# Kernel tuning notes

Hardware: AMD Instinct MI355X
Metric: run time of the kernel (lower is better)

## Reference

```python
import jax, jax.numpy as jnp
import numpy as np
import math

H = 128      # hidden_channels
R = 32       # num_rbf
N = 4096     # atoms
E = 65536    # edges
CU = 4.5     # cutoff_upper (cutoff_lower = 0)
ALPHA = 5.0 / CU
MEANS = jnp.linspace(math.exp(-CU), 1.0, R, dtype=jnp.float32)
BETA = jnp.float32((2.0 / R * (1.0 - math.exp(-CU))) ** -2)
EPS = 1e-5


def _ln(x, g, b):
    mu = x.mean(-1, keepdims=True)
    var = ((x - mu) ** 2).mean(-1, keepdims=True)
    return (x - mu) * jax.lax.rsqrt(var + EPS) * g + b


def setup_inputs() -> dict:
    key = jax.random.key(0)
    ks = jax.random.split(key, 20)
    f32 = jnp.float32

    def w(i, shape):
        return jax.random.normal(ks[i], shape, f32) / np.float32(np.sqrt(shape[-1]))

    return {
        "edge_vec": jax.random.normal(ks[0], (E, 3), f32) * 1.5,
        "emb_w": w(1, (128, H)),
        "emb2_w": w(2, (H, 2 * H)), "emb2_b": jnp.zeros((H,), f32),
        "dp1_w": w(3, (H, R)), "dp1_b": jnp.zeros((H,), f32),
        "dp2_w": w(4, (H, R)), "dp2_b": jnp.zeros((H,), f32),
        "dp3_w": w(5, (H, R)), "dp3_b": jnp.zeros((H,), f32),
        "lt0_w": w(6, (H, H)), "lt1_w": w(7, (H, H)), "lt2_w": w(8, (H, H)),
        "ls0_w": w(9, (2 * H, H)), "ls0_b": jnp.zeros((2 * H,), f32),
        "ls1_w": w(10, (3 * H, 2 * H)), "ls1_b": jnp.zeros((3 * H,), f32),
        "init_g": jnp.ones((H,), f32), "init_b": jnp.zeros((H,), f32),
        "lin_w": w(11, (H, 3 * H)), "lin_b": jnp.zeros((H,), f32),
        "outn_g": jnp.ones((3 * H,), f32), "outn_b": jnp.zeros((3 * H,), f32),
        "ol1_w": w(12, (H // 2, H)), "ol1_b": jnp.zeros((H // 2,), f32),
        "ol2_w": w(13, (1, H // 2)), "ol2_b": jnp.zeros((1,), f32),
        "z": jax.random.randint(ks[14], (N,), 0, 128, dtype=jnp.int32),
        "edge_index": jax.random.randint(ks[15], (2, E), 0, N, dtype=jnp.int32),
    }


def reference(edge_vec, emb_w, emb2_w, emb2_b, dp1_w, dp1_b, dp2_w, dp2_b,
              dp3_w, dp3_b, lt0_w, lt1_w, lt2_w, ls0_w, ls0_b, ls1_w, ls1_b,
              init_g, init_b, lin_w, lin_b, outn_g, outn_b, ol1_w, ol1_b,
              ol2_w, ol2_b, z, edge_index):
    n = z.shape[0]
    src, dst = edge_index[0], edge_index[1]

    d = jnp.sqrt((edge_vec ** 2).sum(-1))                 # (E,)
    vn = edge_vec / d[:, None]                             # unit edge vectors
    cut = jnp.where(d < CU, 0.5 * (jnp.cos(jnp.pi * d / CU) + 1.0), 0.0)
    # expnorm RBF
    rbf = cut[:, None] * jnp.exp(-BETA * (jnp.exp(-ALPHA * d)[:, None] - MEANS) ** 2)  # (E,R)

    # atomic-number message Zij = emb2(cat(emb(z_i), emb(z_j)))
    zpair = jnp.concatenate([emb_w[z[src]], emb_w[z[dst]]], -1)  # (E,2H)
    zij = zpair @ emb2_w.T + emb2_b                              # (E,H)
    c = cut[:, None] * zij                                       # cutoff * Zij, (E,H)

    w1 = (rbf @ dp1_w.T + dp1_b) * c    # scalar channel weights (E,H)
    w2 = (rbf @ dp2_w.T + dp2_b) * c
    w3 = (rbf @ dp3_w.T + dp3_b) * c

    eye = jnp.eye(3, dtype=edge_vec.dtype)
    zero = jnp.zeros_like(vn[:, 0])
    skew = jnp.stack([zero, -vn[:, 2], vn[:, 1],
                      vn[:, 2], zero, -vn[:, 0],
                      -vn[:, 1], vn[:, 0], zero], 1).reshape(-1, 3, 3)  # (E,3,3)
    outer = vn[:, :, None] * vn[:, None, :]
    sym = outer - ((vn ** 2).sum(-1) / 3.0)[:, None, None] * eye        # traceless sym (E,3,3)

    seg = lambda a: jax.ops.segment_sum(a, src, num_segments=n)
    I0 = seg(w1)[:, :, None, None] * eye                                # (N,H,3,3)
    A0 = seg(w2[:, :, None, None] * skew[:, None, :, :])                # (N,H,3,3)
    S0 = seg(w3[:, :, None, None] * sym[:, None, :, :])                 # (N,H,3,3)

    tn = ((I0 + A0 + S0) ** 2).sum((-2, -1))                            # tensor_norm, (N,H)
    nrm = _ln(tn, init_g, init_b)
    h = jax.nn.silu(nrm @ ls0_w.T + ls0_b)
    scal = jax.nn.silu(h @ ls1_w.T + ls1_b).reshape(n, H, 3)            # per-channel gates

    I1 = jnp.einsum('nhxy,gh->ngxy', I0, lt0_w) * scal[..., 0][..., None, None]
    A1 = jnp.einsum('nhxy,gh->ngxy', A0, lt1_w) * scal[..., 1][..., None, None]
    S1 = jnp.einsum('nhxy,gh->ngxy', S0, lt2_w) * scal[..., 2][..., None, None]

    x = jnp.concatenate([(I1 ** 2).sum((-2, -1)),
                         (A1 ** 2).sum((-2, -1)),
                         (S1 ** 2).sum((-2, -1))], -1)                  # (N,3H)
    x = _ln(x, outn_g, outn_b)
    s1 = x @ lin_w.T + lin_b
    s2 = jax.nn.silu(s1) @ ol1_w.T + ol1_b
    s3 = jax.nn.silu(s2) @ ol2_w.T + ol2_b                              # per-atom energy (N,1)
    return s3
```

## Files before the change

### kernel.cpp

```cpp
#include <hip/hip_runtime.h>
#include <math.h>

#define NH_TOT 524288
#define N_ATOM 4096
#define N_EDGE 65536

typedef __attribute__((ext_vector_type(8))) short bf16x8;
typedef __attribute__((ext_vector_type(4))) float f32x4;

__device__ __forceinline__ unsigned short f2bf(float f) {
    unsigned u = __builtin_bit_cast(unsigned, f);
    unsigned r = (u + 0x7fffu + ((u >> 16) & 1u)) >> 16;
    return (unsigned short)r;
}
__device__ __forceinline__ float silu(float v) { return v / (1.0f + __expf(-v)); }

#define WB_LS1 32768
#define WB_LT0 131072
#define WB_LT1 147456
#define WB_LT2 163840
#define WB_DP  180224

__global__ __launch_bounds__(256) void k_setup(
    const float* __restrict__ emb_w, const float* __restrict__ emb2_w,
    const int* __restrict__ ei,
    const float* __restrict__ ls0_w, const float* __restrict__ ls1_w,
    const float* __restrict__ lt0_w, const float* __restrict__ lt1_w,
    const float* __restrict__ lt2_w,
    const float* __restrict__ dp1_w, const float* __restrict__ dp2_w,
    const float* __restrict__ dp3_w,
    float* __restrict__ U1, float* __restrict__ U2,
    int* __restrict__ cnt, unsigned short* __restrict__ wb) {
    const int bx = blockIdx.x, tid = threadIdx.x;
    if (bx < 64) {
        __shared__ float se[2][128];
        const int t = bx * 2 + (tid >> 7), h = tid & 127, half = tid >> 7;
        se[half][h] = emb_w[t * 128 + h];
        __syncthreads();
        float u1 = 0.f, u2 = 0.f;
        const float* row = emb2_w + h * 256;
#pragma unroll 8
        for (int k = 0; k < 128; k++) {
            u1 += se[half][k] * row[k];
            u2 += se[half][k] * row[128 + k];
        }
        U1[t * 128 + h] = u1;
        U2[t * 128 + h] = u2;
    } else if (bx < 320) {
        const int e = (bx - 64) * 256 + tid;
        atomicAdd(&cnt[ei[e]], 1);
    } else {
        const int base = (bx - 320) * 1024 + tid * 4;
        const float* src;
        int off;
        if (base < 32768)       { src = ls0_w; off = 0; }
        else if (base < 131072) { src = ls1_w; off = 32768; }
        else if (base < 147456) { src = lt0_w; off = 131072; }
        else if (base < 163840) { src = lt1_w; off = 147456; }
        else if (base < 180224) { src = lt2_w; off = 163840; }
        else if (base < 184320) { src = dp1_w; off = 180224; }
        else if (base < 188416) { src = dp2_w; off = 184320; }
        else                    { src = dp3_w; off = 188416; }
        const float4 v = *(const float4*)(src + (base - off));
        unsigned short* o = wb + base;
        o[0] = f2bf(v.x); o[1] = f2bf(v.y); o[2] = f2bf(v.z); o[3] = f2bf(v.w);
    }
}

__global__ __launch_bounds__(256) void k_scan(const int* __restrict__ cnt, int* __restrict__ off) {
    __shared__ int s[256];
    const int t = threadIdx.x;
    int loc[16];
    int run = 0;
#pragma unroll
    for (int i = 0; i < 16; i++) { run += cnt[t * 16 + i]; loc[i] = run; }
    s[t] = run;
    __syncthreads();
    for (int d = 1; d < 256; d <<= 1) {
        const int add = (t >= d) ? s[t - d] : 0;
        __syncthreads();
        s[t] += add;
        __syncthreads();
    }
    const int base = s[t] - run;
    if (t == 0) off[0] = 0;
#pragma unroll
    for (int i = 0; i < 16; i++) off[t * 16 + i + 1] = base + loc[i];
}

__global__ __launch_bounds__(256) void k_edge(
    const float* __restrict__ edge_vec, const int* __restrict__ ei,
    const int* __restrict__ z, const int* __restrict__ off,
    int* __restrict__ cursor,
    unsigned short* __restrict__ rbf_bf, float4* __restrict__ geom,
    int* __restrict__ u2off) {
    const int e = blockIdx.x * 256 + threadIdx.x;
    const int src = ei[e];
    const int pos = off[src] + atomicAdd(&cursor[src], 1);

    const float evx = edge_vec[3 * e + 0];
    const float evy = edge_vec[3 * e + 1];
    const float evz = edge_vec[3 * e + 2];
    const float d = sqrtf(evx * evx + evy * evy + evz * evz);
    const float inv = 1.0f / d;
    const float cut = (d < 4.5f) ? 0.5f * (__cosf(0.6981317007977318f * d) + 1.0f) : 0.0f;
    geom[pos] = make_float4(evx * inv, evy * inv, evz * inv, cut);
    u2off[pos] = z[ei[N_EDGE + e]] << 7;

    const float expd = __expf(-1.1111111111111112f * d);
    const float m0 = 0.011108996538242306f;
    const float dm = (1.0f - m0) * (1.0f / 31.0f);
    const float tb = 0.0625f * (1.0f - m0);
    const float beta = 1.0f / (tb * tb);
    unsigned int rb[16];
#pragma unroll
    for (int r = 0; r < 16; r++) {
        const float df0 = expd - (m0 + (float)(2 * r) * dm);
        const float df1 = expd - (m0 + (float)(2 * r + 1) * dm);
        const unsigned lo = f2bf(cut * __expf(-beta * df0 * df0));
        const unsigned hi = f2bf(cut * __expf(-beta * df1 * df1));
        rb[r] = lo | (hi << 16);
    }
    uint4* dst = (uint4*)(rbf_bf + (size_t)pos * 32);
#pragma unroll
    for (int j = 0; j < 4; j++)
        dst[j] = make_uint4(rb[4 * j], rb[4 * j + 1], rb[4 * j + 2], rb[4 * j + 3]);
}

__global__ __launch_bounds__(256) void k_node(
    const int* __restrict__ z, const int* __restrict__ off,
    const unsigned short* __restrict__ rbf_bf, const float4* __restrict__ geom,
    const int* __restrict__ u2off,
    const float* __restrict__ U1, const float* __restrict__ U2,
    const float* __restrict__ emb2_b,
    const float* __restrict__ dp1_b, const float* __restrict__ dp2_b,
    const float* __restrict__ dp3_b,
    const unsigned short* __restrict__ wb,
    const float* __restrict__ init_g, const float* __restrict__ init_b,
    unsigned short* __restrict__ acc_bf, unsigned short* __restrict__ nrm_bf) {
    const int tid = threadIdx.x;
    const int wave = tid >> 6, lane = tid & 63, lm = lane & 15, lq = lane >> 4;
    const int nb = blockIdx.x * 8;

    const unsigned short* dpw = wb + WB_DP;
    bf16x8 bfr[3][2];
    float bhc[2], bk1[2], bk2[2], bk3[2];
    int cols[2];
#pragma unroll
    for (int t = 0; t < 2; t++) {
        const int col = wave * 32 + t * 16 + lm;
        cols[t] = col;
        bhc[t] = emb2_b[col];
        bk1[t] = dp1_b[col]; bk2[t] = dp2_b[col]; bk3[t] = dp3_b[col];
#pragma unroll
        for (int k = 0; k < 3; k++)
            bfr[k][t] = *(const bf16x8*)(dpw + k * 4096 + col * 32 + lq * 8);
    }

    __shared__ float redS[8][4];
    __shared__ float redQ[8][4];

    float tnA[8], tnB[8];

    for (int nn = 0; nn < 8; nn++) {
        const int n = nb + nn;
        const int beg = off[n];
        const int En = off[n + 1] - beg;
        const int zoff = z[n] << 7;
        const float u1c0 = U1[zoff + cols[0]];
        const float u1c1 = U1[zoff + cols[1]];

        float part[10][2];
#pragma unroll
        for (int p = 0; p < 10; p++) { part[p][0] = 0.f; part[p][1] = 0.f; }

        for (int mi = 0; mi < En; mi += 16) {
            const int arow = beg + min(mi + lm, En - 1);
            const bf16x8 af = *(const bf16x8*)(rbf_bf + (size_t)arow * 32 + lq * 8);
            f32x4 c[3][2];
#pragma unroll
            for (int k = 0; k < 3; k++)
#pragma unroll
                for (int t = 0; t < 2; t++)
                    c[k][t] = __builtin_amdgcn_mfma_f32_16x16x32_bf16(
                        af, bfr[k][t], (f32x4){0.f, 0.f, 0.f, 0.f}, 0, 0, 0);
#pragma unroll
            for (int r = 0; r < 4; r++) {
                const int er = mi + lq * 4 + r;
                const bool valid = er < En;
                const int p = beg + (valid ? er : 0);
                const float4 g = geom[p];
                const int u2o = u2off[p];
#pragma unroll
                for (int t = 0; t < 2; t++) {
                    const float u2v = U2[u2o + cols[t]];
                    const float u1h = (t == 0) ? u1c0 : u1c1;
                    const float cc = valid ? g.w * (u1h + u2v + bhc[t]) : 0.f;
                    const float w1 = (c[0][t][r] + bk1[t]) * cc;
                    const float w2 = (c[1][t][r] + bk2[t]) * cc;
                    const float w3 = (c[2][t][r] + bk3[t]) * cc;
                    part[0][t] += w1;
                    part[1][t] += w2 * g.x; part[2][t] += w2 * g.y; part[3][t] += w2 * g.z;
                    const float tx = w3 * g.x, ty = w3 * g.y;
                    part[4][t] += tx * g.x; part[5][t] += tx * g.y; part[6][t] += tx * g.z;
                    part[7][t] += ty * g.y; part[8][t] += ty * g.z; part[9][t] += w3 * g.z * g.z;
                }
            }
        }

#pragma unroll
        for (int p = 0; p < 10; p++)
#pragma unroll
            for (int t = 0; t < 2; t++) {
                float v = part[p][t];
                v += __shfl_xor(v, 16, 64);
                v += __shfl_xor(v, 32, 64);
                part[p][t] = v;
            }
        if (lq == 0) {
#pragma unroll
            for (int p = 0; p < 10; p++)
#pragma unroll
                for (int t = 0; t < 2; t++)
                    acc_bf[(size_t)p * NH_TOT + n * 128 + cols[t]] = f2bf(part[p][t]);
        }

        float tn[2];
#pragma unroll
        for (int t = 0; t < 2; t++) {
            const float aI = part[0][t];
            const float axv = part[1][t], ayv = part[2][t], azv = part[3][t];
            const float mxx = part[4][t], mxy = part[5][t], mxz = part[6][t];
            const float myy = part[7][t], myz = part[8][t], mzz = part[9][t];
            const float tr3 = (mxx + myy + mzz) * (1.0f / 3.0f);
            const float t00 = aI + mxx - tr3;
            const float t11 = aI + myy - tr3;
            const float t22 = aI + mzz - tr3;
            tn[t] = t00 * t00 + t11 * t11 + t22 * t22 +
                    2.0f * (mxy * mxy + azv * azv + mxz * mxz + ayv * ayv + myz * myz + axv * axv);
        }
        tnA[nn] = tn[0];
        tnB[nn] = tn[1];

        float s = (lq == 0) ? (tn[0] + tn[1]) : 0.f;
        s += __shfl_xor(s, 1, 64);
        s += __shfl_xor(s, 2, 64);
        s += __shfl_xor(s, 4, 64);
        s += __shfl_xor(s, 8, 64);
        if (lane == 0) redS[nn][wave] = s;
    }
    __syncthreads();

    float dvA[8], dvB[8];
#pragma unroll
    for (int nn = 0; nn < 8; nn++) {
        const float mu = (redS[nn][0] + redS[nn][1] + redS[nn][2] + redS[nn][3]) * (1.0f / 128.0f);
        dvA[nn] = tnA[nn] - mu;
        dvB[nn] = tnB[nn] - mu;
        float q = (lq == 0) ? (dvA[nn] * dvA[nn] + dvB[nn] * dvB[nn]) : 0.f;
        q += __shfl_xor(q, 1, 64);
        q += __shfl_xor(q, 2, 64);
        q += __shfl_xor(q, 4, 64);
        q += __shfl_xor(q, 8, 64);
        if (lane == 0) redQ[nn][wave] = q;
    }
    __syncthreads();

    if (lq == 0) {
        const float g0 = init_g[cols[0]], g1 = init_g[cols[1]];
        const float b0 = init_b[cols[0]], b1 = init_b[cols[1]];
#pragma unroll
        for (int nn = 0; nn < 8; nn++) {
            const float var = (redQ[nn][0] + redQ[nn][1] + redQ[nn][2] + redQ[nn][3]) * (1.0f / 128.0f);
            const float rs = rsqrtf(var + 1e-5f);
            const int n = nb + nn;
            nrm_bf[n * 128 + cols[0]] = f2bf(dvA[nn] * rs * g0 + b0);
            nrm_bf[n * 128 + cols[1]] = f2bf(dvB[nn] * rs * g1 + b1);
        }
    }
}

__global__ __launch_bounds__(256) void k_megatail(
    const unsigned short* __restrict__ nrm_bf, const unsigned short* __restrict__ acc_bf,
    const unsigned short* __restrict__ wb,
    const float* __restrict__ ls0_b, const float* __restrict__ ls1_b,
    const float* __restrict__ outn_g, const float* __restrict__ outn_b,
    const float* __restrict__ lin_w, const float* __restrict__ lin_b,
    const float* __restrict__ ol1_w, const float* __restrict__ ol1_b,
    const float* __restrict__ ol2_w, const float* __restrict__ ol2_b,
    float* __restrict__ out) {
    const int tid = threadIdx.x, wave = tid >> 6, lane = tid & 63;
    const int lm = lane & 15, lq = lane >> 4;
    const int n0 = blockIdx.x * 8;

    __shared__ unsigned short h1[16][280];
    __shared__ float scal_s[8][388];
    __shared__ float xs[8][392];
    __shared__ float ss[8][132];

    {
        f32x4 acc[4];
#pragma unroll
        for (int j = 0; j < 4; j++) acc[j] = (f32x4){0.f, 0.f, 0.f, 0.f};
        const int cbase = wave * 64;
#pragma unroll
        for (int kc = 0; kc < 128; kc += 32) {
            const int arow = n0 + min(lm, 7);
            const bf16x8 af = *(const bf16x8*)(nrm_bf + (size_t)arow * 128 + kc + lq * 8);
#pragma unroll
            for (int sn = 0; sn < 4; sn++) {
                const bf16x8 b = *(const bf16x8*)(wb + (size_t)(cbase + sn * 16 + lm) * 128 + kc + lq * 8);
                acc[sn] = __builtin_amdgcn_mfma_f32_16x16x32_bf16(af, b, acc[sn], 0, 0, 0);
            }
        }
#pragma unroll
        for (int sn = 0; sn < 4; sn++) {
            const int col = cbase + sn * 16 + lm;
            const float bv = ls0_b[col];
#pragma unroll
            for (int r = 0; r < 4; r++)
                h1[lq * 4 + r][col] = f2bf(silu(acc[sn][r] + bv));
        }
    }
    __syncthreads();
    {
        f32x4 acc[6];
#pragma unroll
        for (int j = 0; j < 6; j++) acc[j] = (f32x4){0.f, 0.f, 0.f, 0.f};
        const int cbase = wave * 96;
        const unsigned short* ls1p = wb + WB_LS1;
#pragma unroll 2
        for (int kc = 0; kc < 256; kc += 32) {
            const bf16x8 af = *(const bf16x8*)(&h1[lm][kc + lq * 8]);
#pragma unroll
            for (int sn = 0; sn < 6; sn++) {
                const bf16x8 b = *(const bf16x8*)(ls1p + (size_t)(cbase + sn * 16 + lm) * 256 + kc + lq * 8);
                acc[sn] = __builtin_amdgcn_mfma_f32_16x16x32_bf16(af, b, acc[sn], 0, 0, 0);
            }
        }
#pragma unroll
        for (int sn = 0; sn < 6; sn++) {
            const int col = cbase + sn * 16 + lm;
            const float bv = ls1_b[col];
#pragma unroll
            for (int r = 0; r < 4; r++) {
                const int node = lq * 4 + r;
                if (node < 8) scal_s[node][col] = silu(acc[sn][r] + bv);
            }
        }
    }
    __syncthreads();

    f32x4 e0[2], e1[2], e2[2], trv[2];
#pragma unroll
    for (int sn = 0; sn < 2; sn++) {
        e0[sn] = (f32x4){0.f, 0.f, 0.f, 0.f};
        e1[sn] = (f32x4){0.f, 0.f, 0.f, 0.f};
        e2[sn] = (f32x4){0.f, 0.f, 0.f, 0.f};
        trv[sn] = (f32x4){0.f, 0.f, 0.f, 0.f};
    }
#pragma unroll
    for (int p = 0; p < 10; p++) {
        const unsigned short* A = acc_bf + (size_t)p * NH_TOT;
        const unsigned short* B = wb + (p == 0 ? WB_LT0 : (p < 4 ? WB_LT1 : WB_LT2));
        f32x4 c[2];
        c[0] = (f32x4){0.f, 0.f, 0.f, 0.f};
        c[1] = (f32x4){0.f, 0.f, 0.f, 0.f};
#pragma unroll
        for (int kc = 0; kc < 128; kc += 32) {
            const int arow = n0 + min(lm, 7);
            const bf16x8 af = *(const bf16x8*)(A + (size_t)arow * 128 + kc + lq * 8);
#pragma unroll
            for (int sn = 0; sn < 2; sn++) {
                const bf16x8 b = *(const bf16x8*)(B + (size_t)(wave * 32 + sn * 16 + lm) * 128 + kc + lq * 8);
                c[sn] = __builtin_amdgcn_mfma_f32_16x16x32_bf16(af, b, c[sn], 0, 0, 0);
            }
        }
#pragma unroll
        for (int sn = 0; sn < 2; sn++) {
            if (p == 0)      e0[sn] += c[sn] * c[sn];
            else if (p < 4)  e1[sn] += c[sn] * c[sn];
            else if (p == 4 || p == 7 || p == 9) { e2[sn] += c[sn] * c[sn]; trv[sn] += c[sn]; }
            else             e2[sn] += 2.0f * c[sn] * c[sn];
        }
    }

    if (lq < 2) {
#pragma unroll
        for (int sn = 0; sn < 2; sn++) {
            const int g = wave * 32 + sn * 16 + lm;
#pragma unroll
            for (int r = 0; r < 4; r++) {
                const int node = lq * 4 + r;
                const float s0 = scal_s[node][3 * g + 0];
                const float s1 = scal_s[node][3 * g + 1];
                const float s2 = scal_s[node][3 * g + 2];
                xs[node][g]       = 3.0f * e0[sn][r] * s0 * s0;
                xs[node][128 + g] = 2.0f * e1[sn][r] * s1 * s1;
                const float tr = trv[sn][r];
                xs[node][256 + g] = (e2[sn][r] - tr * tr * (1.0f / 3.0f)) * s2 * s2;
            }
        }
    }
    __syncthreads();

#pragma unroll
    for (int i = 0; i < 2; i++) {
        const int node = wave * 2 + i;
        float v[6];
        float s = 0.f;
#pragma unroll
        for (int j = 0; j < 6; j++) { v[j] = xs[node][lane + 64 * j]; s += v[j]; }
#pragma unroll
        for (int o = 1; o < 64; o <<= 1) s += __shfl_xor(s, o, 64);
        const float mu = s * (1.0f / 384.0f);
        float q = 0.f;
#pragma unroll
        for (int j = 0; j < 6; j++) { v[j] -= mu; q += v[j] * v[j]; }
#pragma unroll
        for (int o = 1; o < 64; o <<= 1) q += __shfl_xor(q, o, 64);
        const float rs = rsqrtf(q * (1.0f / 384.0f) + 1e-5f);
#pragma unroll
        for (int j = 0; j < 6; j++) {
            const int col = lane + 64 * j;
            xs[node][col] = v[j] * rs * outn_g[col] + outn_b[col];
        }
    }
    __syncthreads();

    {
        const int j = tid & 127, half = tid >> 7;
        float a4[4];
        const float lb = lin_b[j];
#pragma unroll
        for (int i = 0; i < 4; i++) a4[i] = lb;
        const float4* wr = (const float4*)(lin_w + j * 384);
#pragma unroll 2
        for (int k4 = 0; k4 < 96; k4++) {
            const float4 w4 = wr[k4];
#pragma unroll
            for (int i = 0; i < 4; i++) {
                const float4 xv = *(const float4*)&xs[half * 4 + i][k4 * 4];
                a4[i] += w4.x * xv.x + w4.y * xv.y + w4.z * xv.z + w4.w * xv.w;
            }
        }
#pragma unroll
        for (int i = 0; i < 4; i++) ss[half * 4 + i][j] = silu(a4[i]);
    }
    __syncthreads();

    {
        const int o = tid & 63, q = tid >> 6;
        float a2v[2];
        const float ob = ol1_b[o];
        a2v[0] = ob; a2v[1] = ob;
        const float4* o4 = (const float4*)(ol1_w + o * 128);
#pragma unroll 4
        for (int k4 = 0; k4 < 32; k4++) {
            const float4 w4 = o4[k4];
#pragma unroll
            for (int i = 0; i < 2; i++) {
                const float4 sv = *(const float4*)&ss[q * 2 + i][k4 * 4];
                a2v[i] += w4.x * sv.x + w4.y * sv.y + w4.z * sv.z + w4.w * sv.w;
            }
        }
        const float w2 = ol2_w[o];
#pragma unroll
        for (int i = 0; i < 2; i++) {
            float v = silu(a2v[i]) * w2;
            for (int s = 32; s > 0; s >>= 1) v += __shfl_down(v, s, 64);
            if (o == 0) out[n0 + q * 2 + i] = v + ol2_b[0];
        }
    }
}

extern "C" void kernel_launch(void* const* d_in, const int* in_sizes, int n_in,
                              void* d_out, int out_size, void* d_ws, size_t ws_size,
                              hipStream_t stream) {
    (void)in_sizes; (void)n_in; (void)out_size; (void)ws_size;
    const float* edge_vec = (const float*)d_in[0];
    const float* emb_w   = (const float*)d_in[1];
    const float* emb2_w  = (const float*)d_in[2];
    const float* emb2_b  = (const float*)d_in[3];
    const float* dp1_w   = (const float*)d_in[4];
    const float* dp1_b   = (const float*)d_in[5];
    const float* dp2_w   = (const float*)d_in[6];
    const float* dp2_b   = (const float*)d_in[7];
    const float* dp3_w   = (const float*)d_in[8];
    const float* dp3_b   = (const float*)d_in[9];
    const float* lt0_w   = (const float*)d_in[10];
    const float* lt1_w   = (const float*)d_in[11];
    const float* lt2_w   = (const float*)d_in[12];
    const float* ls0_w   = (const float*)d_in[13];
    const float* ls0_b   = (const float*)d_in[14];
    const float* ls1_w   = (const float*)d_in[15];
    const float* ls1_b   = (const float*)d_in[16];
    const float* init_g  = (const float*)d_in[17];
    const float* init_b  = (const float*)d_in[18];
    const float* lin_w   = (const float*)d_in[19];
    const float* lin_b   = (const float*)d_in[20];
    const float* outn_g  = (const float*)d_in[21];
    const float* outn_b  = (const float*)d_in[22];
    const float* ol1_w   = (const float*)d_in[23];
    const float* ol1_b   = (const float*)d_in[24];
    const float* ol2_w   = (const float*)d_in[25];
    const float* ol2_b   = (const float*)d_in[26];
    const int* z  = (const int*)d_in[27];
    const int* ei = (const int*)d_in[28];
    float* out = (float*)d_out;

    char* w = (char*)d_ws;
    int*            cnt    = (int*)(w);
    int*            cursor = (int*)(w + 16384);
    int*            off    = (int*)(w + 32768);
    unsigned short* wb     = (unsigned short*)(w + 49408);
    float*          U1     = (float*)(w + 434432);
    float*          U2     = (float*)(w + 499968);
    int*            u2off  = (int*)(w + 565504);
    float4*         geom   = (float4*)(w + 827648);
    unsigned short* rbf_bf = (unsigned short*)(w + 1876224);
    unsigned short* nrm_bf = (unsigned short*)(w + 6070528);
    unsigned short* acc_bf = (unsigned short*)(w + 7119104);

    hipMemsetAsync(w, 0, 32768, stream);
    k_setup<<<dim3(508), dim3(256), 0, stream>>>(emb_w, emb2_w, ei,
                                                 ls0_w, ls1_w, lt0_w, lt1_w, lt2_w,
                                                 dp1_w, dp2_w, dp3_w,
                                                 U1, U2, cnt, wb);
    k_scan<<<dim3(1), dim3(256), 0, stream>>>(cnt, off);
    k_edge<<<dim3(256), dim3(256), 0, stream>>>(edge_vec, ei, z, off, cursor,
                                                rbf_bf, geom, u2off);
    k_node<<<dim3(512), dim3(256), 0, stream>>>(z, off, rbf_bf, geom, u2off, U1, U2,
                                                emb2_b, dp1_b, dp2_b, dp3_b, wb,
                                                init_g, init_b, acc_bf, nrm_bf);
    k_megatail<<<dim3(512), dim3(256), 0, stream>>>(nrm_bf, acc_bf, wb, ls0_b, ls1_b,
                                                    outn_g, outn_b, lin_w, lin_b,
                                                    ol1_w, ol1_b, ol2_w, ol2_b, out);
}
```

Measured before the change: 246.5 us.

## Fuse edge RBF/geometry computation into node kernel and parallelize embedding matmul

Replaces the edge kernel, which wrote bf16 RBF rows, geometry and neighbor offsets to global memory, with a small scatter kernel that only records a sorted edge order. The node kernel now recomputes distance, cutoff, unit vector and the RBF fragment per lane in registers and shares geometry across lanes with shuffles, which cuts global memory traffic and a full pass over the edges. The U1/U2 embedding product is split into one wave per output with a shuffle reduction instead of serial 128-long loops. The node kernel handles 4 atoms per block instead of 8, doubling the grid. In exchange the node kernel does more exp work per edge and makes gathered reads of edge_vec and z.

Result: faster. 237.7 us (-3.6%).

```diff
diff --git a/kernel.cpp b/kernel.cpp
--- a/kernel.cpp
+++ b/kernel.cpp
@@ -32,25 +32,31 @@
     float* __restrict__ U1, float* __restrict__ U2,
     int* __restrict__ cnt, unsigned short* __restrict__ wb) {
     const int bx = blockIdx.x, tid = threadIdx.x;
-    if (bx < 64) {
-        __shared__ float se[2][128];
-        const int t = bx * 2 + (tid >> 7), h = tid & 127, half = tid >> 7;
-        se[half][h] = emb_w[t * 128 + h];
-        __syncthreads();
-        float u1 = 0.f, u2 = 0.f;
+    if (bx < 4096) {
+        const int idx = bx * 4 + (tid >> 6);
+        const int t = idx >> 7, h = idx & 127;
+        const int lane = tid & 63;
+        const float e0 = emb_w[t * 128 + lane];
+        const float e1 = emb_w[t * 128 + 64 + lane];
         const float* row = emb2_w + h * 256;
-#pragma unroll 8
-        for (int k = 0; k < 128; k++) {
-            u1 += se[half][k] * row[k];
-            u2 += se[half][k] * row[128 + k];
-        }
-        U1[t * 128 + h] = u1;
-        U2[t * 128 + h] = u2;
-    } else if (bx < 320) {
-        const int e = (bx - 64) * 256 + tid;
+        const float w0 = row[lane], w1 = row[64 + lane];
+        const float w2 = row[128 + lane], w3 = row[192 + lane];
+        float u1 = e0 * w0 + e1 * w1;
+        float u2 = e0 * w2 + e1 * w3;
+#pragma unroll
+        for (int o = 1; o < 64; o <<= 1) {
+            u1 += __shfl_xor(u1, o, 64);
+            u2 += __shfl_xor(u2, o, 64);
+        }
+        if (lane == 0) {
+            U1[t * 128 + h] = u1;
+            U2[t * 128 + h] = u2;
+        }
+    } else if (bx < 4352) {
+        const int e = (bx - 4096) * 256 + tid;
         atomicAdd(&cnt[ei[e]], 1);
     } else {
-        const int base = (bx - 320) * 1024 + tid * 4;
+        const int base = (bx - 4352) * 1024 + tid * 4;
         const float* src;
         int off;
         if (base < 32768)       { src = ls0_w; off = 0; }
@@ -88,49 +94,19 @@
     for (int i = 0; i < 16; i++) off[t * 16 + i + 1] = base + loc[i];
 }
 
-__global__ __launch_bounds__(256) void k_edge(
-    const float* __restrict__ edge_vec, const int* __restrict__ ei,
-    const int* __restrict__ z, const int* __restrict__ off,
-    int* __restrict__ cursor,
-    unsigned short* __restrict__ rbf_bf, float4* __restrict__ geom,
-    int* __restrict__ u2off) {
+__global__ __launch_bounds__(256) void k_scatter(const int* __restrict__ ei,
+                                                 const int* __restrict__ off,
+                                                 int* __restrict__ cursor,
+                                                 int* __restrict__ order) {
     const int e = blockIdx.x * 256 + threadIdx.x;
-    const int src = ei[e];
-    const int pos = off[src] + atomicAdd(&cursor[src], 1);
-
-    const float evx = edge_vec[3 * e + 0];
-    const float evy = edge_vec[3 * e + 1];
-    const float evz = edge_vec[3 * e + 2];
-    const float d = sqrtf(evx * evx + evy * evy + evz * evz);
-    const float inv = 1.0f / d;
-    const float cut = (d < 4.5f) ? 0.5f * (__cosf(0.6981317007977318f * d) + 1.0f) : 0.0f;
-    geom[pos] = make_float4(evx * inv, evy * inv, evz * inv, cut);
-    u2off[pos] = z[ei[N_EDGE + e]] << 7;
-
-    const float expd = __expf(-1.1111111111111112f * d);
-    const float m0 = 0.011108996538242306f;
-    const float dm = (1.0f - m0) * (1.0f / 31.0f);
-    const float tb = 0.0625f * (1.0f - m0);
-    const float beta = 1.0f / (tb * tb);
-    unsigned int rb[16];
-#pragma unroll
-    for (int r = 0; r < 16; r++) {
-        const float df0 = expd - (m0 + (float)(2 * r) * dm);
-        const float df1 = expd - (m0 + (float)(2 * r + 1) * dm);
-        const unsigned lo = f2bf(cut * __expf(-beta * df0 * df0));
-        const unsigned hi = f2bf(cut * __expf(-beta * df1 * df1));
-        rb[r] = lo | (hi << 16);
-    }
-    uint4* dst = (uint4*)(rbf_bf + (size_t)pos * 32);
-#pragma unroll
-    for (int j = 0; j < 4; j++)
-        dst[j] = make_uint4(rb[4 * j], rb[4 * j + 1], rb[4 * j + 2], rb[4 * j + 3]);
+    const int s = ei[e];
+    order[off[s] + atomicAdd(&cursor[s], 1)] = e;
 }
 
 __global__ __launch_bounds__(256) void k_node(
     const int* __restrict__ z, const int* __restrict__ off,
-    const unsigned short* __restrict__ rbf_bf, const float4* __restrict__ geom,
-    const int* __restrict__ u2off,
+    const int* __restrict__ order, const int* __restrict__ ei,
+    const float* __restrict__ edge_vec,
     const float* __restrict__ U1, const float* __restrict__ U2,
     const float* __restrict__ emb2_b,
     const float* __restrict__ dp1_b, const float* __restrict__ dp2_b,
@@ -140,7 +116,7 @@
     unsigned short* __restrict__ acc_bf, unsigned short* __restrict__ nrm_bf) {
     const int tid = threadIdx.x;
     const int wave = tid >> 6, lane = tid & 63, lm = lane & 15, lq = lane >> 4;
-    const int nb = blockIdx.x * 8;
+    const int nb = blockIdx.x * 4;
 
     const unsigned short* dpw = wb + WB_DP;
     bf16x8 bfr[3][2];
@@ -157,12 +133,18 @@
             bfr[k][t] = *(const bf16x8*)(dpw + k * 4096 + col * 32 + lq * 8);
     }
 
-    __shared__ float redS[8][4];
-    __shared__ float redQ[8][4];
-
-    float tnA[8], tnB[8];
-
-    for (int nn = 0; nn < 8; nn++) {
+    const float m0 = 0.011108996538242306f;
+    const float dm = (1.0f - m0) * (1.0f / 31.0f);
+    const float tb = 0.0625f * (1.0f - m0);
+    const float beta = 1.0f / (tb * tb);
+    const float mean0 = m0 + (float)(lq * 8) * dm;
+
+    __shared__ float redS[4][4];
+    __shared__ float redQ[4][4];
+
+    float tnA[4], tnB[4];
+
+    for (int nn = 0; nn < 4; nn++) {
         const int n = nb + nn;
         const int beg = off[n];
         const int En = off[n + 1] - beg;
@@ -175,8 +157,25 @@
         for (int p = 0; p < 10; p++) { part[p][0] = 0.f; part[p][1] = 0.f; }
 
         for (int mi = 0; mi < En; mi += 16) {
-            const int arow = beg + min(mi + lm, En - 1);
-            const bf16x8 af = *(const bf16x8*)(rbf_bf + (size_t)arow * 32 + lq * 8);
+            const int e = order[beg + min(mi + lm, En - 1)];
+            const float evx = edge_vec[3 * e + 0];
+            const float evy = edge_vec[3 * e + 1];
+            const float evz = edge_vec[3 * e + 2];
+            const float d = sqrtf(evx * evx + evy * evy + evz * evz);
+            const float inv = 1.0f / d;
+            const float cut = (d < 4.5f) ? 0.5f * (__cosf(0.6981317007977318f * d) + 1.0f) : 0.0f;
+            const float vx = evx * inv, vy = evy * inv, vz = evz * inv;
+            const int u2o = z[ei[N_EDGE + e]] << 7;
+            const float expd = __expf(-1.1111111111111112f * d);
+
+            union { bf16x8 v; unsigned short s[8]; } uf;
+#pragma unroll
+            for (int j = 0; j < 8; j++) {
+                const float df = expd - (mean0 + (float)j * dm);
+                uf.s[j] = f2bf(cut * __expf(-beta * df * df));
+            }
+            const bf16x8 af = uf.v;
+
             f32x4 c[3][2];
 #pragma unroll
             for (int k = 0; k < 3; k++)
@@ -184,26 +183,30 @@
                 for (int t = 0; t < 2; t++)
                     c[k][t] = __builtin_amdgcn_mfma_f32_16x16x32_bf16(
                         af, bfr[k][t], (f32x4){0.f, 0.f, 0.f, 0.f}, 0, 0, 0);
+
 #pragma unroll
             for (int r = 0; r < 4; r++) {
                 const int er = mi + lq * 4 + r;
                 const bool valid = er < En;
-                const int p = beg + (valid ? er : 0);
-                const float4 g = geom[p];
-                const int u2o = u2off[p];
+                const int sl = (lane & 48) | (lq * 4 + r);
+                const float gvx = __shfl(vx, sl, 64);
+                const float gvy = __shfl(vy, sl, 64);
+                const float gvz = __shfl(vz, sl, 64);
+                const float gct = __shfl(cut, sl, 64);
+                const int   go  = __shfl(u2o, sl, 64);
 #pragma unroll
                 for (int t = 0; t < 2; t++) {
-                    const float u2v = U2[u2o + cols[t]];
+                    const float u2v = U2[go + cols[t]];
                     const float u1h = (t == 0) ? u1c0 : u1c1;
-                    const float cc = valid ? g.w * (u1h + u2v + bhc[t]) : 0.f;
+                    const float cc = valid ? gct * (u1h + u2v + bhc[t]) : 0.f;
                     const float w1 = (c[0][t][r] + bk1[t]) * cc;
                     const float w2 = (c[1][t][r] + bk2[t]) * cc;
                     const float w3 = (c[2][t][r] + bk3[t]) * cc;
                     part[0][t] += w1;
-                    part[1][t] += w2 * g.x; part[2][t] += w2 * g.y; part[3][t] += w2 * g.z;
-                    const float tx = w3 * g.x, ty = w3 * g.y;
-                    part[4][t] += tx * g.x; part[5][t] += tx * g.y; part[6][t] += tx * g.z;
-                    part[7][t] += ty * g.y; part[8][t] += ty * g.z; part[9][t] += w3 * g.z * g.z;
+                    part[1][t] += w2 * gvx; part[2][t] += w2 * gvy; part[3][t] += w2 * gvz;
+                    const float tx = w3 * gvx, ty = w3 * gvy;
+                    part[4][t] += tx * gvx; part[5][t] += tx * gvy; part[6][t] += tx * gvz;
+                    part[7][t] += ty * gvy; part[8][t] += ty * gvz; part[9][t] += w3 * gvz * gvz;
                 }
             }
         }
@@ -251,9 +254,9 @@
     }
     __syncthreads();
 
-    float dvA[8], dvB[8];
-#pragma unroll
-    for (int nn = 0; nn < 8; nn++) {
+    float dvA[4], dvB[4];
+#pragma unroll
+    for (int nn = 0; nn < 4; nn++) {
         const float mu = (redS[nn][0] + redS[nn][1] + redS[nn][2] + redS[nn][3]) * (1.0f / 128.0f);
         dvA[nn] = tnA[nn] - mu;
         dvB[nn] = tnB[nn] - mu;
@@ -270,7 +273,7 @@
         const float g0 = init_g[cols[0]], g1 = init_g[cols[1]];
         const float b0 = init_b[cols[0]], b1 = init_b[cols[1]];
 #pragma unroll
-        for (int nn = 0; nn < 8; nn++) {
+        for (int nn = 0; nn < 4; nn++) {
             const float var = (redQ[nn][0] + redQ[nn][1] + redQ[nn][2] + redQ[nn][3]) * (1.0f / 128.0f);
             const float rs = rsqrtf(var + 1e-5f);
             const int n = nb + nn;
@@ -516,23 +519,20 @@
     unsigned short* wb     = (unsigned short*)(w + 49408);
     float*          U1     = (float*)(w + 434432);
     float*          U2     = (float*)(w + 499968);
-    int*            u2off  = (int*)(w + 565504);
-    float4*         geom   = (float4*)(w + 827648);
-    unsigned short* rbf_bf = (unsigned short*)(w + 1876224);
-    unsigned short* nrm_bf = (unsigned short*)(w + 6070528);
-    unsigned short* acc_bf = (unsigned short*)(w + 7119104);
+    int*            order  = (int*)(w + 565504);
+    unsigned short* nrm_bf = (unsigned short*)(w + 827648);
+    unsigned short* acc_bf = (unsigned short*)(w + 1876224);
 
     hipMemsetAsync(w, 0, 32768, stream);
-    k_setup<<<dim3(508), dim3(256), 0, stream>>>(emb_w, emb2_w, ei,
-                                                 ls0_w, ls1_w, lt0_w, lt1_w, lt2_w,
-                                                 dp1_w, dp2_w, dp3_w,
-                                                 U1, U2, cnt, wb);
+    k_setup<<<dim3(4540), dim3(256), 0, stream>>>(emb_w, emb2_w, ei,
+                                                  ls0_w, ls1_w, lt0_w, lt1_w, lt2_w,
+                                                  dp1_w, dp2_w, dp3_w,
+                                                  U1, U2, cnt, wb);
     k_scan<<<dim3(1), dim3(256), 0, stream>>>(cnt, off);
-    k_edge<<<dim3(256), dim3(256), 0, stream>>>(edge_vec, ei, z, off, cursor,
-                                                rbf_bf, geom, u2off);
-    k_node<<<dim3(512), dim3(256), 0, stream>>>(z, off, rbf_bf, geom, u2off, U1, U2,
-                                                emb2_b, dp1_b, dp2_b, dp3_b, wb,
-                                                init_g, init_b, acc_bf, nrm_bf);
+    k_scatter<<<dim3(256), dim3(256), 0, stream>>>(ei, off, cursor, order);
+    k_node<<<dim3(1024), dim3(256), 0, stream>>>(z, off, order, ei, edge_vec, U1, U2,
+                                                 emb2_b, dp1_b, dp2_b, dp3_b, wb,
+                                                 init_g, init_b, acc_bf, nrm_bf);
     k_megatail<<<dim3(512), dim3(256), 0, stream>>>(nrm_bf, acc_bf, wb, ls0_b, ls1_b,
                                                     outn_g, outn_b, lin_w, lin_b,
                                                     ol1_w, ol1_b, ol2_w, ol2_b, out);
```
